# Kernel optimization log

Measured on AMD Instinct MI355X. Metric: run time of the kernel, lower is better.

## Reference

```python
import jax, jax.numpy as jnp
import numpy as np


def setup_inputs() -> dict:
    key = jax.random.key(0)
    inputs = jax.random.normal(key, (32, 8192, 128), dtype=jnp.float32)
    return {"inputs": inputs}


def reference(inputs):
    # Per-batch covariance, matching tfp.stats.covariance defaults:
    # sample_axis=0 (here axis 1 per batch item), event_axis=-1, divide by N.
    n = inputs.shape[1]
    mean = jnp.mean(inputs, axis=1, keepdims=True)          # [B, 1, D]
    xc = inputs - mean                                       # [B, N, D]
    cov = jnp.einsum('bnd,bne->bde', xc, xc) / n             # [B, D, D]
    return cov
```

## Files before the change

### kernel.cpp

```cpp
#include <hip/hip_runtime.h>

#define D_DIM 128
#define N_DIM 8192
#define B_DIM 32
#define BK 64

typedef float f32x4 __attribute__((ext_vector_type(4)));
typedef short bf16x8 __attribute__((ext_vector_type(8)));
typedef unsigned short u16;

__device__ __forceinline__ u16 f2bf(float f) {
    unsigned int u = __builtin_bit_cast(unsigned int, f);
    u += 0x7FFFu + ((u >> 16) & 1u);
    return (u16)(u >> 16);
}

__global__ __launch_bounds__(256, 2) void cov_partial(
    const float* __restrict__ in, float* __restrict__ ws_p,
    float* __restrict__ ws_s, int kc) {
    __shared__ u16 lds[D_DIM * BK];
    __shared__ float red[8][D_DIM];

    const int t    = threadIdx.x;
    const int b    = blockIdx.y;
    const int ks   = blockIdx.x;
    const int dc   = t >> 3;
    const int nr   = t & 7;
    const int wv   = t >> 6;
    const int lane = t & 63;
    const int m    = lane & 15;
    const int q    = lane >> 4;

    const int nstep = kc / BK;
    const float* src = in + (size_t)b * (N_DIM * D_DIM) + (size_t)ks * kc * D_DIM;

    f32x4 acc[2][8];
#pragma unroll
    for (int r = 0; r < 2; ++r)
#pragma unroll
        for (int c = 0; c < 8; ++c) acc[r][c] = (f32x4)0.0f;

    float sum4[4] = {0.f, 0.f, 0.f, 0.f};

    f32x4 buf[8];
    {
        const float* p = src;
#pragma unroll
        for (int sub = 0; sub < 2; ++sub)
#pragma unroll
            for (int i = 0; i < 4; ++i)
                buf[sub * 4 + i] =
                    *(const f32x4*)(p + (size_t)(sub * 32 + 4 * nr + i) * D_DIM + 4 * dc);
    }

    for (int s = 0; s < nstep; ++s) {
#pragma unroll
        for (int x = 0; x < 8; ++x)
#pragma unroll
            for (int j = 0; j < 4; ++j) sum4[j] += buf[x][j];

        ushort4 wvreg[2][4];
#pragma unroll
        for (int sub = 0; sub < 2; ++sub)
#pragma unroll
            for (int j = 0; j < 4; ++j) {
                wvreg[sub][j].x = f2bf(buf[sub * 4 + 0][j]);
                wvreg[sub][j].y = f2bf(buf[sub * 4 + 1][j]);
                wvreg[sub][j].z = f2bf(buf[sub * 4 + 2][j]);
                wvreg[sub][j].w = f2bf(buf[sub * 4 + 3][j]);
            }

        if (s + 1 < nstep) {
            const float* p = src + (size_t)(s + 1) * BK * D_DIM;
#pragma unroll
            for (int sub = 0; sub < 2; ++sub)
#pragma unroll
                for (int i = 0; i < 4; ++i)
                    buf[sub * 4 + i] =
                        *(const f32x4*)(p + (size_t)(sub * 32 + 4 * nr + i) * D_DIM + 4 * dc);
        }

        __syncthreads();
#pragma unroll
        for (int sub = 0; sub < 2; ++sub)
#pragma unroll
            for (int j = 0; j < 4; ++j) {
                int d = 4 * dc + j;
                int g = sub * 4 + (nr >> 1);
                int slot = g ^ (d & 7);
                int off = d * 64 + slot * 8 + 4 * (nr & 1);
                *(ushort4*)(lds + off) = wvreg[sub][j];
            }
        __syncthreads();

#pragma unroll
        for (int h = 0; h < 2; ++h) {
            bf16x8 Fcol[8];
#pragma unroll
            for (int tt = 0; tt < 8; ++tt) {
                int slot = (4 * h + q) ^ (m & 7);
                Fcol[tt] = *(const bf16x8*)(lds + (16 * tt + m) * 64 + slot * 8);
            }
            bf16x8 Frow[2];
#pragma unroll
            for (int r = 0; r < 2; ++r) {
                int row = 32 * wv + 16 * r + m;
                int slot = (4 * h + q) ^ (m & 7);
                Frow[r] = *(const bf16x8*)(lds + row * 64 + slot * 8);
            }
#pragma unroll
            for (int r = 0; r < 2; ++r)
#pragma unroll
                for (int c = 0; c < 8; ++c)
                    acc[r][c] = __builtin_amdgcn_mfma_f32_16x16x32_bf16(
                        Frow[r], Fcol[c], acc[r][c], 0, 0, 0);
        }
    }

#pragma unroll
    for (int j = 0; j < 4; ++j) red[nr][4 * dc + j] = sum4[j];
    __syncthreads();
    if (t < D_DIM) {
        float ssum = 0.f;
#pragma unroll
        for (int i = 0; i < 8; ++i) ssum += red[i][t];
        ws_s[(size_t)(b * gridDim.x + ks) * D_DIM + t] = ssum;
    }

    f32x4* outv = (f32x4*)(ws_p + (size_t)(b * gridDim.x + ks) * (D_DIM * D_DIM));
#pragma unroll
    for (int r = 0; r < 2; ++r)
#pragma unroll
        for (int c = 0; c < 8; ++c)
            outv[t * 16 + r * 8 + c] = acc[r][c];
}

__global__ __launch_bounds__(256) void cov_reduce(
    const float* __restrict__ ws_p, const float* __restrict__ ws_s,
    float* __restrict__ out, int kspl) {
    int b = blockIdx.x >> 4;
    int chunk = blockIdx.x & 15;
    int g = chunk * 256 + threadIdx.x;

    __shared__ float mean[D_DIM];
    if (threadIdx.x < D_DIM) {
        float s = 0.f;
        for (int ks = 0; ks < kspl; ++ks)
            s += ws_s[(size_t)(b * kspl + ks) * D_DIM + threadIdx.x];
        mean[threadIdx.x] = s * (1.0f / (float)N_DIM);
    }
    __syncthreads();

    const f32x4* pv = (const f32x4*)ws_p;
    f32x4 acc = (f32x4)0.0f;
    for (int ks = 0; ks < kspl; ++ks) {
        f32x4 v = pv[(size_t)(b * kspl + ks) * (D_DIM * D_DIM / 4) + g];
        acc.x += v.x; acc.y += v.y; acc.z += v.z; acc.w += v.w;
    }

    int t2 = g >> 4;
    int rc = g & 15;
    int r = rc >> 3, c = rc & 7;
    int wv = t2 >> 6;
    int lane = t2 & 63;
    int m = lane & 15;
    int q = lane >> 4;
    int d0 = 32 * wv + 16 * r + 4 * q;
    int e = 16 * c + m;

    const float invN = 1.0f / (float)N_DIM;
    float me = mean[e];
    float* ob = out + (size_t)b * (D_DIM * D_DIM);
#pragma unroll
    for (int i = 0; i < 4; ++i) {
        int d = d0 + i;
        ob[(size_t)d * D_DIM + e] = acc[i] * invN - mean[d] * me;
    }
}

extern "C" void kernel_launch(void* const* d_in, const int* in_sizes, int n_in,
                              void* d_out, int out_size, void* d_ws, size_t ws_size,
                              hipStream_t stream) {
    const float* in = (const float*)d_in[0];
    float* out = (float*)d_out;

    int kspl = 16;
    while (kspl > 1 &&
           (size_t)kspl * B_DIM * (size_t)(D_DIM * D_DIM + D_DIM) * sizeof(float) > ws_size)
        kspl >>= 1;
    int kc = N_DIM / kspl;

    float* ws_p = (float*)d_ws;
    float* ws_s = ws_p + (size_t)kspl * B_DIM * (D_DIM * D_DIM);

    cov_partial<<<dim3(kspl, B_DIM), 256, 0, stream>>>(in, ws_p, ws_s, kc);
    cov_reduce<<<dim3(B_DIM * 16), 256, 0, stream>>>(ws_p, ws_s, out, kspl);
}
```

Measured before the change: 207.6 us.

## Stage 256-row bf16 tiles in LDS with double-buffered loads and fewer barriers

The LDS tile grows from 64 to 256 rows. Each block now runs two big MFMA phases instead of eight small ones, with two register buffers alternating global loads against conversion and LDS writes. The goal is to cut __syncthreads count and keep more global loads in flight. In exchange, LDS use rises to 64KB per block, which may limit occupancy, and the hardcoded KSPL=16 drops the workspace-size fallback.

Measured after the change: 208.6 us. About the same (+0.5%).

```diff
diff --git a/kernel.cpp b/kernel.cpp
--- a/kernel.cpp
+++ b/kernel.cpp
@@ -3,7 +3,9 @@
 #define D_DIM 128
 #define N_DIM 8192
 #define B_DIM 32
-#define BK 64
+#define KSPL 16
+#define KC   512
+#define BK   256
 
 typedef float f32x4 __attribute__((ext_vector_type(4)));
 typedef short bf16x8 __attribute__((ext_vector_type(8)));
@@ -15,9 +17,70 @@
     return (u16)(u >> 16);
 }
 
+__device__ __forceinline__ void load_chunk(f32x4 (&buf)[8], const float* src,
+                                           int gc, int nr, int dc) {
+    const float* p = src + (size_t)gc * 64 * D_DIM;
+#pragma unroll
+    for (int sub = 0; sub < 2; ++sub)
+#pragma unroll
+        for (int i = 0; i < 4; ++i)
+            buf[sub * 4 + i] =
+                *(const f32x4*)(p + (size_t)(sub * 32 + 4 * nr + i) * D_DIM + 4 * dc);
+}
+
+__device__ __forceinline__ void proc_write(u16* lds, f32x4 (&buf)[8],
+                                           float (&sum4)[4], int gc, int nr, int dc) {
+#pragma unroll
+    for (int x = 0; x < 8; ++x)
+#pragma unroll
+        for (int j = 0; j < 4; ++j) sum4[j] += buf[x][j];
+#pragma unroll
+    for (int sub = 0; sub < 2; ++sub)
+#pragma unroll
+        for (int j = 0; j < 4; ++j) {
+            ushort4 w;
+            w.x = f2bf(buf[sub * 4 + 0][j]);
+            w.y = f2bf(buf[sub * 4 + 1][j]);
+            w.z = f2bf(buf[sub * 4 + 2][j]);
+            w.w = f2bf(buf[sub * 4 + 3][j]);
+            int d = 4 * dc + j;
+            int g = (gc & 3) * 8 + sub * 4 + (nr >> 1);
+            int slot = g ^ (d & 7);
+            *(ushort4*)(lds + d * 256 + slot * 8 + 4 * (nr & 1)) = w;
+        }
+}
+
+__device__ __forceinline__ void mfma_phase(const u16* lds, f32x4 (&acc)[2][8],
+                                           int wv, int m, int q) {
+#pragma unroll
+    for (int h = 0; h < 8; ++h) {
+        int slotbase = h * 4 + q;
+        bf16x8 Fcol[8];
+#pragma unroll
+        for (int tt = 0; tt < 8; ++tt) {
+            int slot = slotbase ^ (m & 7);
+            Fcol[tt] = *(const bf16x8*)(lds + (16 * tt + m) * 256 + slot * 8);
+        }
+        bf16x8 Frow0, Frow1;
+        {
+            int slot = slotbase ^ (m & 7);
+            Frow0 = *(const bf16x8*)(lds + (32 * wv + m) * 256 + slot * 8);
+            Frow1 = *(const bf16x8*)(lds + (32 * wv + 16 + m) * 256 + slot * 8);
+        }
+#pragma unroll
+        for (int c = 0; c < 8; ++c)
+            acc[0][c] = __builtin_amdgcn_mfma_f32_16x16x32_bf16(Frow0, Fcol[c],
+                                                                acc[0][c], 0, 0, 0);
+#pragma unroll
+        for (int c = 0; c < 8; ++c)
+            acc[1][c] = __builtin_amdgcn_mfma_f32_16x16x32_bf16(Frow1, Fcol[c],
+                                                                acc[1][c], 0, 0, 0);
+    }
+}
+
 __global__ __launch_bounds__(256, 2) void cov_partial(
     const float* __restrict__ in, float* __restrict__ ws_p,
-    float* __restrict__ ws_s, int kc) {
+    float* __restrict__ ws_s) {
     __shared__ u16 lds[D_DIM * BK];
     __shared__ float red[8][D_DIM];
 
@@ -31,92 +94,41 @@
     const int m    = lane & 15;
     const int q    = lane >> 4;
 
-    const int nstep = kc / BK;
-    const float* src = in + (size_t)b * (N_DIM * D_DIM) + (size_t)ks * kc * D_DIM;
+    const float* src = in + (size_t)b * (N_DIM * D_DIM) + (size_t)ks * KC * D_DIM;
 
     f32x4 acc[2][8];
 #pragma unroll
     for (int r = 0; r < 2; ++r)
 #pragma unroll
         for (int c = 0; c < 8; ++c) acc[r][c] = (f32x4)0.0f;
-
     float sum4[4] = {0.f, 0.f, 0.f, 0.f};
 
-    f32x4 buf[8];
-    {
-        const float* p = src;
-#pragma unroll
-        for (int sub = 0; sub < 2; ++sub)
-#pragma unroll
-            for (int i = 0; i < 4; ++i)
-                buf[sub * 4 + i] =
-                    *(const f32x4*)(p + (size_t)(sub * 32 + 4 * nr + i) * D_DIM + 4 * dc);
-    }
-
-    for (int s = 0; s < nstep; ++s) {
-#pragma unroll
-        for (int x = 0; x < 8; ++x)
-#pragma unroll
-            for (int j = 0; j < 4; ++j) sum4[j] += buf[x][j];
-
-        ushort4 wvreg[2][4];
-#pragma unroll
-        for (int sub = 0; sub < 2; ++sub)
-#pragma unroll
-            for (int j = 0; j < 4; ++j) {
-                wvreg[sub][j].x = f2bf(buf[sub * 4 + 0][j]);
-                wvreg[sub][j].y = f2bf(buf[sub * 4 + 1][j]);
-                wvreg[sub][j].z = f2bf(buf[sub * 4 + 2][j]);
-                wvreg[sub][j].w = f2bf(buf[sub * 4 + 3][j]);
-            }
-
-        if (s + 1 < nstep) {
-            const float* p = src + (size_t)(s + 1) * BK * D_DIM;
-#pragma unroll
-            for (int sub = 0; sub < 2; ++sub)
-#pragma unroll
-                for (int i = 0; i < 4; ++i)
-                    buf[sub * 4 + i] =
-                        *(const f32x4*)(p + (size_t)(sub * 32 + 4 * nr + i) * D_DIM + 4 * dc);
-        }
-
-        __syncthreads();
-#pragma unroll
-        for (int sub = 0; sub < 2; ++sub)
-#pragma unroll
-            for (int j = 0; j < 4; ++j) {
-                int d = 4 * dc + j;
-                int g = sub * 4 + (nr >> 1);
-                int slot = g ^ (d & 7);
-                int off = d * 64 + slot * 8 + 4 * (nr & 1);
-                *(ushort4*)(lds + off) = wvreg[sub][j];
-            }
-        __syncthreads();
-
-#pragma unroll
-        for (int h = 0; h < 2; ++h) {
-            bf16x8 Fcol[8];
-#pragma unroll
-            for (int tt = 0; tt < 8; ++tt) {
-                int slot = (4 * h + q) ^ (m & 7);
-                Fcol[tt] = *(const bf16x8*)(lds + (16 * tt + m) * 64 + slot * 8);
-            }
-            bf16x8 Frow[2];
-#pragma unroll
-            for (int r = 0; r < 2; ++r) {
-                int row = 32 * wv + 16 * r + m;
-                int slot = (4 * h + q) ^ (m & 7);
-                Frow[r] = *(const bf16x8*)(lds + row * 64 + slot * 8);
-            }
-#pragma unroll
-            for (int r = 0; r < 2; ++r)
-#pragma unroll
-                for (int c = 0; c < 8; ++c)
-                    acc[r][c] = __builtin_amdgcn_mfma_f32_16x16x32_bf16(
-                        Frow[r], Fcol[c], acc[r][c], 0, 0, 0);
-        }
-    }
-
+    f32x4 bufA[8], bufB[8];
+
+    load_chunk(bufA, src, 0, nr, dc);
+    load_chunk(bufB, src, 1, nr, dc);
+    proc_write(lds, bufA, sum4, 0, nr, dc);
+    load_chunk(bufA, src, 2, nr, dc);
+    proc_write(lds, bufB, sum4, 1, nr, dc);
+    load_chunk(bufB, src, 3, nr, dc);
+    proc_write(lds, bufA, sum4, 2, nr, dc);
+    load_chunk(bufA, src, 4, nr, dc);
+    proc_write(lds, bufB, sum4, 3, nr, dc);
+    __syncthreads();
+    mfma_phase(lds, acc, wv, m, q);
+    __syncthreads();
+
+    load_chunk(bufB, src, 5, nr, dc);
+    proc_write(lds, bufA, sum4, 4, nr, dc);
+    load_chunk(bufA, src, 6, nr, dc);
+    proc_write(lds, bufB, sum4, 5, nr, dc);
+    load_chunk(bufB, src, 7, nr, dc);
+    proc_write(lds, bufA, sum4, 6, nr, dc);
+    proc_write(lds, bufB, sum4, 7, nr, dc);
+    __syncthreads();
+    mfma_phase(lds, acc, wv, m, q);
+
+    __syncthreads();
 #pragma unroll
     for (int j = 0; j < 4; ++j) red[nr][4 * dc + j] = sum4[j];
     __syncthreads();
@@ -124,10 +136,10 @@
         float ssum = 0.f;
 #pragma unroll
         for (int i = 0; i < 8; ++i) ssum += red[i][t];
-        ws_s[(size_t)(b * gridDim.x + ks) * D_DIM + t] = ssum;
-    }
-
-    f32x4* outv = (f32x4*)(ws_p + (size_t)(b * gridDim.x + ks) * (D_DIM * D_DIM));
+        ws_s[(size_t)(b * KSPL + ks) * D_DIM + t] = ssum;
+    }
+
+    f32x4* outv = (f32x4*)(ws_p + (size_t)(b * KSPL + ks) * (D_DIM * D_DIM));
 #pragma unroll
     for (int r = 0; r < 2; ++r)
 #pragma unroll
@@ -184,15 +196,9 @@
     const float* in = (const float*)d_in[0];
     float* out = (float*)d_out;
 
-    int kspl = 16;
-    while (kspl > 1 &&
-           (size_t)kspl * B_DIM * (size_t)(D_DIM * D_DIM + D_DIM) * sizeof(float) > ws_size)
-        kspl >>= 1;
-    int kc = N_DIM / kspl;
-
     float* ws_p = (float*)d_ws;
-    float* ws_s = ws_p + (size_t)kspl * B_DIM * (D_DIM * D_DIM);
-
-    cov_partial<<<dim3(kspl, B_DIM), 256, 0, stream>>>(in, ws_p, ws_s, kc);
-    cov_reduce<<<dim3(B_DIM * 16), 256, 0, stream>>>(ws_p, ws_s, out, kspl);
-}
+    float* ws_s = ws_p + (size_t)KSPL * B_DIM * (D_DIM * D_DIM);
+
+    cov_partial<<<dim3(KSPL, B_DIM), 256, 0, stream>>>(in, ws_p, ws_s);
+    cov_reduce<<<dim3(B_DIM * 16), 256, 0, stream>>>(ws_p, ws_s, out, KSPL);
+}
```
